# Kernel tuning notes

Hardware: AMD Instinct MI355X
Metric: run time of the kernel (lower is better)

## Reference

```python
import jax
import jax.numpy as jnp
import numpy as np

DEPTH = 8
CODEBOOK_SIZE = 1024
EMBED_DIM = 256
N_TOKENS = 131072


def setup_inputs() -> dict:
    key = jax.random.key(0)
    k_lat, k_cb = jax.random.split(key)
    latent = jax.random.normal(k_lat, (N_TOKENS, EMBED_DIM), dtype=jnp.float32)
    # matches torch.randn(depth, K, D) * 0.02 initialization
    codebooks = jax.random.normal(k_cb, (DEPTH, CODEBOOK_SIZE, EMBED_DIM), dtype=jnp.float32) * 0.02
    return {"latent": latent, "codebooks": codebooks}


def reference(latent, codebooks):
    """Residual VQ: per level, squared-L2 nearest codeword, gather, residual update.

    latent:    [N, D]
    codebooks: [depth, K, D]
    returns (straight_through [N, D], codes [depth, N] int32)
    """

    def step(carry, cb):
        residual, qsum = carry  # [N, D], [N, D]
        # ||r||^2 - 2 r.c + ||c||^2  -> [N, K]
        dist = (
            jnp.sum(residual * residual, axis=-1, keepdims=True)
            - 2.0 * jnp.einsum("nd,kd->nk", residual, cb)
            + jnp.sum(cb * cb, axis=-1)[None, :]
        )
        idx = jnp.argmin(dist, axis=1)  # [N]
        quantized = cb[idx]  # [N, D]
        return (residual - quantized, qsum + quantized), idx

    init = (latent, jnp.zeros_like(latent))
    (_, quantized_sum), codes = jax.lax.scan(step, init, codebooks)
    straight_through = latent + jax.lax.stop_gradient(quantized_sum - latent)
    return straight_through, codes
```

## Files before the change

### kernel.cpp

```cpp
#include <hip/hip_runtime.h>


#define NTOK 131072
#define DEPTH 8
#define KCB 1024
#define DIM 256
#define TM 16
#define RP 260
#define RBP 264
#define WWIN 0.12f
#define ALARM 0.05f
#define LCAP 64

typedef __attribute__((ext_vector_type(8))) short short8v;
typedef __attribute__((ext_vector_type(4))) float f32x4;

__device__ __forceinline__ unsigned short f32_to_bf16_rne(float f) {
  unsigned int u = __float_as_uint(f);
  return (unsigned short)((u + 0x7FFFu + ((u >> 16) & 1u)) >> 16);
}

__device__ __forceinline__ unsigned int fkey(float f) {
  unsigned int b = __float_as_uint(f);
  return (b & 0x80000000u) ? ~b : (b | 0x80000000u);
}
__device__ __forceinline__ float finv(unsigned int k) {
  return (k & 0x80000000u) ? __uint_as_float(k ^ 0x80000000u)
                           : __uint_as_float(~k);
}

__device__ __forceinline__ float np_sumsq_128(const float* p) {
  float s[16];
#pragma unroll
  for (int l = 0; l < 16; ++l) {
    float r0 = __fadd_rn(__fmul_rn(p[l], p[l]),
                         __fmul_rn(p[l + 64], p[l + 64]));
    float r1 = __fadd_rn(__fmul_rn(p[l + 16], p[l + 16]),
                         __fmul_rn(p[l + 80], p[l + 80]));
    float r2 = __fadd_rn(__fmul_rn(p[l + 32], p[l + 32]),
                         __fmul_rn(p[l + 96], p[l + 96]));
    float r3 = __fadd_rn(__fmul_rn(p[l + 48], p[l + 48]),
                         __fmul_rn(p[l + 112], p[l + 112]));
    s[l] = __fadd_rn(__fadd_rn(r0, r1), __fadd_rn(r2, r3));
  }
  float t[8];
#pragma unroll
  for (int l = 0; l < 8; ++l) t[l] = __fadd_rn(s[l], s[l + 8]);
  float u[4];
#pragma unroll
  for (int l = 0; l < 4; ++l) u[l] = __fadd_rn(t[l], t[l + 4]);
  return __fadd_rn(__fadd_rn(u[0], u[2]), __fadd_rn(u[1], u[3]));
}

__device__ __forceinline__ float np_sumsq_256(const float* p) {
  return __fadd_rn(np_sumsq_128(p), np_sumsq_128(p + 128));
}

__device__ __forceinline__ float np_sumsq_256_par(const float* p, int kc) {
  float half[2];
#pragma unroll
  for (int h = 0; h < 2; ++h) {
    const float* q = p + h * 128;
    float r0 = __fadd_rn(__fmul_rn(q[kc], q[kc]),
                         __fmul_rn(q[kc + 64], q[kc + 64]));
    float r1 = __fadd_rn(__fmul_rn(q[kc + 16], q[kc + 16]),
                         __fmul_rn(q[kc + 80], q[kc + 80]));
    float r2 = __fadd_rn(__fmul_rn(q[kc + 32], q[kc + 32]),
                         __fmul_rn(q[kc + 96], q[kc + 96]));
    float r3 = __fadd_rn(__fmul_rn(q[kc + 48], q[kc + 48]),
                         __fmul_rn(q[kc + 112], q[kc + 112]));
    float s = __fadd_rn(__fadd_rn(r0, r1), __fadd_rn(r2, r3));
    float t = __fadd_rn(s, __shfl_down(s, 8, 16));
    float u = __fadd_rn(t, __shfl_down(t, 4, 16));
    float v = __fadd_rn(u, __shfl_down(u, 2, 16));
    half[h] = __fadd_rn(v, __shfl_down(v, 1, 16));
  }
  return __fadd_rn(half[0], half[1]);
}

__device__ __forceinline__ float np_dist(const float* rrow, const float* crow,
                                         float A, float C) {
  float dot = 0.f;
#pragma unroll 8
  for (int q = 0; q < 64; ++q) {
    float4 rv = *(const float4*)(rrow + q * 4);
    float4 cv = *(const float4*)(crow + q * 4);
    dot = fmaf(rv.x, cv.x, dot);
    dot = fmaf(rv.y, cv.y, dot);
    dot = fmaf(rv.z, cv.z, dot);
    dot = fmaf(rv.w, cv.w, dot);
  }
  return __fadd_rn(__fsub_rn(A, __fmul_rn(2.0f, dot)), C);
}

__global__ __launch_bounds__(256) void c2_kernel(const float* __restrict__ cbs,
                                                 float* __restrict__ C32g) {
  int gid = blockIdx.x * 256 + threadIdx.x;
  C32g[gid] = np_sumsq_256(cbs + (size_t)gid * DIM);
}

__global__ __launch_bounds__(256) void pack_kernel(
    const float* __restrict__ cbs, unsigned short* __restrict__ cbf) {
  int gid = blockIdx.x * 256 + threadIdx.x;
  int lane = gid & 63;
  int s = (gid >> 6) & 7;
  int g = (gid >> 9) & 63;
  int lvl = gid >> 15;
  int kcol = g * 16 + (lane & 15);
  int kd0 = s * 32 + (lane >> 4) * 8;
  const float* src = cbs + ((size_t)lvl * KCB + kcol) * DIM + kd0;
  unsigned short t[8];
#pragma unroll
  for (int j = 0; j < 8; ++j) t[j] = f32_to_bf16_rne(src[j]);
  ushort4 lo = {t[0], t[1], t[2], t[3]};
  ushort4 hi = {t[4], t[5], t[6], t[7]};
  *(ushort4*)(cbf + (size_t)gid * 8) = lo;
  *(ushort4*)(cbf + (size_t)gid * 8 + 4) = hi;
}

__global__ __launch_bounds__(256, 6) void rvq_kernel(
    const float* __restrict__ latent, const float* __restrict__ cbs,
    const float* __restrict__ C32g, const unsigned short* __restrict__ cbf,
    float* __restrict__ out) {
  __shared__ float r_m[TM][RP];
  __shared__ __align__(16) unsigned short rb[TM * RBP];
  __shared__ float A_s[TM];
  __shared__ unsigned int gkey[TM];
  __shared__ int cnt[TM];
  __shared__ int list[TM][LCAP];
  __shared__ int idx_s[TM];

  const int tid = threadIdx.x;
  const int w = tid >> 6;
  const int lane = tid & 63;
  const int lc = lane & 15;
  const int lg = lane >> 4;
  const int n0 = blockIdx.x * TM;

  {
    int tok = tid >> 4;
    int db = (tid & 15) * 16;
    const float* src = latent + (size_t)(n0 + tok) * DIM + db;
#pragma unroll
    for (int j = 0; j < 4; ++j) {
      float4 v = *(const float4*)(src + j * 4);
      *(float4*)&r_m[tok][db + j * 4] = v;
      rb[tok * RBP + db + j * 4 + 0] = f32_to_bf16_rne(v.x);
      rb[tok * RBP + db + j * 4 + 1] = f32_to_bf16_rne(v.y);
      rb[tok * RBP + db + j * 4 + 2] = f32_to_bf16_rne(v.z);
      rb[tok * RBP + db + j * 4 + 3] = f32_to_bf16_rne(v.w);
    }
    if (tid < TM) {
      gkey[tid] = 0xFFFFFFFFu;
      cnt[tid] = 0;
    }
  }
  __syncthreads();

  for (int lvl = 0; lvl < DEPTH; ++lvl) {
    const float* cb = cbs + (size_t)lvl * KCB * DIM;

    {
      float A = np_sumsq_256_par(&r_m[tid >> 4][0], tid & 15);
      if ((tid & 15) == 0) A_s[tid >> 4] = A;
    }

#pragma unroll 1
    for (int p = 0; p < 4; ++p) {
      f32x4 acc[4];
#pragma unroll
      for (int nt = 0; nt < 4; ++nt) acc[nt] = (f32x4){0.f, 0.f, 0.f, 0.f};

      const int kt0 = p * 16 + w * 4;
      const unsigned short* bp0 =
          cbf + ((((size_t)lvl * 64 + kt0) * 8) * 64 + lane) * 8;
      short8v a0c = *(const short8v*)&rb[lc * RBP + lg * 8];
      short8v b0c = *(const short8v*)(bp0 + 0 * 4096);
      short8v b1c = *(const short8v*)(bp0 + 1 * 4096);
      short8v b2c = *(const short8v*)(bp0 + 2 * 4096);
      short8v b3c = *(const short8v*)(bp0 + 3 * 4096);
#pragma unroll
      for (int s = 0; s < 8; ++s) {
        short8v a0n, b0n, b1n, b2n, b3n;
        if (s < 7) {
          a0n = *(const short8v*)&rb[lc * RBP + (s + 1) * 32 + lg * 8];
          const unsigned short* bs = bp0 + (size_t)(s + 1) * 512;
          b0n = *(const short8v*)(bs + 0 * 4096);
          b1n = *(const short8v*)(bs + 1 * 4096);
          b2n = *(const short8v*)(bs + 2 * 4096);
          b3n = *(const short8v*)(bs + 3 * 4096);
        }
        acc[0] = __builtin_amdgcn_mfma_f32_16x16x32_bf16(a0c, b0c, acc[0], 0, 0, 0);
        acc[1] = __builtin_amdgcn_mfma_f32_16x16x32_bf16(a0c, b1c, acc[1], 0, 0, 0);
        acc[2] = __builtin_amdgcn_mfma_f32_16x16x32_bf16(a0c, b2c, acc[2], 0, 0, 0);
        acc[3] = __builtin_amdgcn_mfma_f32_16x16x32_bf16(a0c, b3c, acc[3], 0, 0, 0);
        if (s < 7) {
          a0c = a0n;
          b0c = b0n;
          b1c = b1n;
          b2c = b2n;
          b3c = b3n;
        }
      }

      float tmin[4];
#pragma unroll
      for (int reg = 0; reg < 4; ++reg) tmin[reg] = 3.4e38f;
#pragma unroll
      for (int nt = 0; nt < 4; ++nt) {
        float Cv = C32g[lvl * KCB + (kt0 + nt) * 16 + lc];
        f32x4 sc;
#pragma unroll
        for (int reg = 0; reg < 4; ++reg) {
          float v = __fsub_rn(Cv, __fmul_rn(2.0f, acc[nt][reg]));
          sc[reg] = v;
          tmin[reg] = fminf(tmin[reg], v);
        }
        acc[nt] = sc;
      }
#pragma unroll
      for (int m = 1; m <= 8; m <<= 1)
#pragma unroll
        for (int reg = 0; reg < 4; ++reg)
          tmin[reg] = fminf(tmin[reg], __shfl_xor(tmin[reg], m));
      if (lc == 0) {
#pragma unroll
        for (int reg = 0; reg < 4; ++reg)
          atomicMin(&gkey[lg * 4 + reg], fkey(tmin[reg]));
      }
#pragma unroll
      for (int reg = 0; reg < 4; ++reg) {
        int t = lg * 4 + reg;
        float th = finv(gkey[t]) + WWIN;
#pragma unroll
        for (int nt = 0; nt < 4; ++nt) {
          if (acc[nt][reg] <= th) {
            int slot = atomicAdd(&cnt[t], 1);
            if (slot < LCAP) list[t][slot] = (kt0 + nt) * 16 + lc;
          }
        }
      }
    }
    __syncthreads();

    {
      int t = tid >> 4;
      int kc = tid & 15;
      float A = A_s[t];
      float gminf = finv(gkey[t]);
      int n = cnt[t];
      float bd = 3.4e38f;
      int bk = KCB;
      if (n <= LCAP) {
        for (int ci = kc; ci < n; ci += 16) {
          int k = list[t][ci];
          float d = np_dist(&r_m[t][0], cb + (size_t)k * DIM, A,
                            C32g[lvl * KCB + k]);
          if (d < bd || (d == bd && k < bk)) {
            bd = d;
            bk = k;
          }
        }
      }
#pragma unroll
      for (int m = 1; m <= 8; m <<= 1) {
        float od = __shfl_xor(bd, m);
        int ok = __shfl_xor(bk, m);
        if (od < bd || (od == bd && ok < bk)) {
          bd = od;
          bk = ok;
        }
      }
      bool redo =
          (n > LCAP) || (fabsf(__fsub_rn(bd, A) - gminf) > (WWIN - ALARM));
      if (redo) {
        bd = 3.4e38f;
        bk = KCB;
        for (int k = kc; k < KCB; k += 16) {
          float d = np_dist(&r_m[t][0], cb + (size_t)k * DIM, A,
                            C32g[lvl * KCB + k]);
          if (d < bd || (d == bd && k < bk)) {
            bd = d;
            bk = k;
          }
        }
#pragma unroll
        for (int m = 1; m <= 8; m <<= 1) {
          float od = __shfl_xor(bd, m);
          int ok = __shfl_xor(bk, m);
          if (od < bd || (od == bd && ok < bk)) {
            bd = od;
            bk = ok;
          }
        }
      }
      if (kc == 0) {
        idx_s[t] = bk;
        out[(size_t)NTOK * DIM + (size_t)lvl * NTOK + n0 + t] = (float)bk;
      }
    }
    __syncthreads();

    {
      int tok = tid >> 4;
      int db = (tid & 15) * 16;
      const float* crow = cb + (size_t)idx_s[tok] * DIM + db;
#pragma unroll
      for (int j = 0; j < 4; ++j) {
        float4 cv4 = *(const float4*)(crow + j * 4);
        int d = db + j * 4;
        float x0 = __fsub_rn(r_m[tok][d + 0], cv4.x);
        float x1 = __fsub_rn(r_m[tok][d + 1], cv4.y);
        float x2 = __fsub_rn(r_m[tok][d + 2], cv4.z);
        float x3 = __fsub_rn(r_m[tok][d + 3], cv4.w);
        r_m[tok][d + 0] = x0;
        r_m[tok][d + 1] = x1;
        r_m[tok][d + 2] = x2;
        r_m[tok][d + 3] = x3;
        rb[tok * RBP + d + 0] = f32_to_bf16_rne(x0);
        rb[tok * RBP + d + 1] = f32_to_bf16_rne(x1);
        rb[tok * RBP + d + 2] = f32_to_bf16_rne(x2);
        rb[tok * RBP + d + 3] = f32_to_bf16_rne(x3);
      }
      if (tid < TM) {
        gkey[tid] = 0xFFFFFFFFu;
        cnt[tid] = 0;
      }
    }
    __syncthreads();
  }

  {
    int tok = tid >> 4;
    int db = (tid & 15) * 16;
#pragma unroll
    for (int j = 0; j < 4; ++j) {
      int d = db + j * 4;
      size_t gi = (size_t)(n0 + tok) * DIM + d;
      float4 l4 = *(const float4*)(latent + gi);
      float4 qv;
      float q;
      q = __fsub_rn(l4.x, r_m[tok][d + 0]);
      qv.x = __fadd_rn(l4.x, __fsub_rn(q, l4.x));
      q = __fsub_rn(l4.y, r_m[tok][d + 1]);
      qv.y = __fadd_rn(l4.y, __fsub_rn(q, l4.y));
      q = __fsub_rn(l4.z, r_m[tok][d + 2]);
      qv.z = __fadd_rn(l4.z, __fsub_rn(q, l4.z));
      q = __fsub_rn(l4.w, r_m[tok][d + 3]);
      qv.w = __fadd_rn(l4.w, __fsub_rn(q, l4.w));
      *(float4*)(out + gi) = qv;
    }
  }
}

extern "C" void kernel_launch(void* const* d_in, const int* in_sizes, int n_in,
                              void* d_out, int out_size, void* d_ws,
                              size_t ws_size, hipStream_t stream) {
  const float* latent = (const float*)d_in[0];
  const float* codebooks = (const float*)d_in[1];
  float* out = (float*)d_out;
  float* C32g = (float*)d_ws;
  unsigned short* cbf = (unsigned short*)((char*)d_ws + 32768);

  hipLaunchKernelGGL(c2_kernel, dim3(DEPTH * KCB / 256), dim3(256), 0, stream,
                     codebooks, C32g);
  hipLaunchKernelGGL(pack_kernel, dim3(DEPTH * 64 * 8 * 64 / 256), dim3(256),
                     0, stream, codebooks, cbf);
  hipLaunchKernelGGL(rvq_kernel, dim3(NTOK / TM), dim3(256), 0, stream, latent,
                     codebooks, C32g, cbf, out);
}
```

Measured before the change: 2.002 ms.

## Enlarge token tile to 64 and keep bf16 residual fragments in registers

Each block now handles 64 tokens, one 16-token row tile per wave, and each wave sweeps the whole codebook. Before, each wave covered a quarter of the codebook for 16 tokens. Every bf16 codebook fragment loaded from global memory now feeds four times as many tokens, which cuts codebook traffic per token. The shared bf16 residual buffer is removed, and each wave converts its A fragments from the fp32 residual straight into registers once per level. In exchange, occupancy drops (launch bounds go from 6 to 4), register pressure rises from the eight persistent A fragments, and the candidate list cap is reduced to 24, which may send more tokens to the overflow fallback path.

```diff
diff --git a/kernel.cpp b/kernel.cpp
--- a/kernel.cpp
+++ b/kernel.cpp
@@ -5,12 +5,11 @@
 #define DEPTH 8
 #define KCB 1024
 #define DIM 256
-#define TM 16
+#define TM 64
 #define RP 260
-#define RBP 264
 #define WWIN 0.12f
 #define ALARM 0.05f
-#define LCAP 64
+#define LCAP 24
 
 typedef __attribute__((ext_vector_type(8))) short short8v;
 typedef __attribute__((ext_vector_type(4))) float f32x4;
@@ -118,12 +117,11 @@
   *(ushort4*)(cbf + (size_t)gid * 8 + 4) = hi;
 }
 
-__global__ __launch_bounds__(256, 6) void rvq_kernel(
+__global__ __launch_bounds__(256, 4) void rvq_kernel(
     const float* __restrict__ latent, const float* __restrict__ cbs,
     const float* __restrict__ C32g, const unsigned short* __restrict__ cbf,
     float* __restrict__ out) {
   __shared__ float r_m[TM][RP];
-  __shared__ __align__(16) unsigned short rb[TM * RBP];
   __shared__ float A_s[TM];
   __shared__ unsigned int gkey[TM];
   __shared__ int cnt[TM];
@@ -136,20 +134,15 @@
   const int lc = lane & 15;
   const int lg = lane >> 4;
   const int n0 = blockIdx.x * TM;
+  const int mrow = w * 16 + lc;
 
   {
-    int tok = tid >> 4;
-    int db = (tid & 15) * 16;
-    const float* src = latent + (size_t)(n0 + tok) * DIM + db;
-#pragma unroll
-    for (int j = 0; j < 4; ++j) {
-      float4 v = *(const float4*)(src + j * 4);
-      *(float4*)&r_m[tok][db + j * 4] = v;
-      rb[tok * RBP + db + j * 4 + 0] = f32_to_bf16_rne(v.x);
-      rb[tok * RBP + db + j * 4 + 1] = f32_to_bf16_rne(v.y);
-      rb[tok * RBP + db + j * 4 + 2] = f32_to_bf16_rne(v.z);
-      rb[tok * RBP + db + j * 4 + 3] = f32_to_bf16_rne(v.w);
-    }
+    int tok = tid >> 2;
+    int part = tid & 3;
+    const float* src = latent + (size_t)(n0 + tok) * DIM + part * 64;
+#pragma unroll
+    for (int j = 0; j < 16; ++j)
+      *(float4*)&r_m[tok][part * 64 + j * 4] = *(const float4*)(src + j * 4);
     if (tid < TM) {
       gkey[tid] = 0xFFFFFFFFu;
       cnt[tid] = 0;
@@ -160,42 +153,57 @@
   for (int lvl = 0; lvl < DEPTH; ++lvl) {
     const float* cb = cbs + (size_t)lvl * KCB * DIM;
 
-    {
-      float A = np_sumsq_256_par(&r_m[tid >> 4][0], tid & 15);
-      if ((tid & 15) == 0) A_s[tid >> 4] = A;
-    }
+#pragma unroll
+    for (int tb = 0; tb < 4; ++tb) {
+      int t = tb * 16 + (tid >> 4);
+      float A = np_sumsq_256_par(&r_m[t][0], tid & 15);
+      if ((tid & 15) == 0) A_s[t] = A;
+    }
+
+    short8v afr[8];
+#pragma unroll
+    for (int s = 0; s < 8; ++s) {
+      unsigned short tmp[8];
+#pragma unroll
+      for (int j = 0; j < 8; ++j)
+        tmp[j] = f32_to_bf16_rne(r_m[mrow][s * 32 + lg * 8 + j]);
+      afr[s] = (short8v){(short)tmp[0], (short)tmp[1], (short)tmp[2],
+                         (short)tmp[3], (short)tmp[4], (short)tmp[5],
+                         (short)tmp[6], (short)tmp[7]};
+    }
+
+    const unsigned short* bp = cbf + (size_t)lvl * 262144 + lane * 8;
+    f32x4 acc[4];
+#pragma unroll
+    for (int nt = 0; nt < 4; ++nt) acc[nt] = (f32x4){0.f, 0.f, 0.f, 0.f};
+    short8v b0c = *(const short8v*)(bp + 0 * 4096);
+    short8v b1c = *(const short8v*)(bp + 1 * 4096);
+    short8v b2c = *(const short8v*)(bp + 2 * 4096);
+    short8v b3c = *(const short8v*)(bp + 3 * 4096);
 
 #pragma unroll 1
-    for (int p = 0; p < 4; ++p) {
-      f32x4 acc[4];
-#pragma unroll
-      for (int nt = 0; nt < 4; ++nt) acc[nt] = (f32x4){0.f, 0.f, 0.f, 0.f};
-
-      const int kt0 = p * 16 + w * 4;
-      const unsigned short* bp0 =
-          cbf + ((((size_t)lvl * 64 + kt0) * 8) * 64 + lane) * 8;
-      short8v a0c = *(const short8v*)&rb[lc * RBP + lg * 8];
-      short8v b0c = *(const short8v*)(bp0 + 0 * 4096);
-      short8v b1c = *(const short8v*)(bp0 + 1 * 4096);
-      short8v b2c = *(const short8v*)(bp0 + 2 * 4096);
-      short8v b3c = *(const short8v*)(bp0 + 3 * 4096);
+    for (int pass = 0; pass < 16; ++pass) {
 #pragma unroll
       for (int s = 0; s < 8; ++s) {
-        short8v a0n, b0n, b1n, b2n, b3n;
-        if (s < 7) {
-          a0n = *(const short8v*)&rb[lc * RBP + (s + 1) * 32 + lg * 8];
-          const unsigned short* bs = bp0 + (size_t)(s + 1) * 512;
-          b0n = *(const short8v*)(bs + 0 * 4096);
-          b1n = *(const short8v*)(bs + 1 * 4096);
-          b2n = *(const short8v*)(bs + 2 * 4096);
-          b3n = *(const short8v*)(bs + 3 * 4096);
-        }
-        acc[0] = __builtin_amdgcn_mfma_f32_16x16x32_bf16(a0c, b0c, acc[0], 0, 0, 0);
-        acc[1] = __builtin_amdgcn_mfma_f32_16x16x32_bf16(a0c, b1c, acc[1], 0, 0, 0);
-        acc[2] = __builtin_amdgcn_mfma_f32_16x16x32_bf16(a0c, b2c, acc[2], 0, 0, 0);
-        acc[3] = __builtin_amdgcn_mfma_f32_16x16x32_bf16(a0c, b3c, acc[3], 0, 0, 0);
-        if (s < 7) {
-          a0c = a0n;
+        short8v b0n, b1n, b2n, b3n;
+        const bool pf = (s < 7) || (pass < 15);
+        if (pf) {
+          const unsigned short* bn =
+              (s < 7) ? (bp + (s + 1) * 512) : (bp + 16384);
+          b0n = *(const short8v*)(bn + 0 * 4096);
+          b1n = *(const short8v*)(bn + 1 * 4096);
+          b2n = *(const short8v*)(bn + 2 * 4096);
+          b3n = *(const short8v*)(bn + 3 * 4096);
+        }
+        acc[0] =
+            __builtin_amdgcn_mfma_f32_16x16x32_bf16(afr[s], b0c, acc[0], 0, 0, 0);
+        acc[1] =
+            __builtin_amdgcn_mfma_f32_16x16x32_bf16(afr[s], b1c, acc[1], 0, 0, 0);
+        acc[2] =
+            __builtin_amdgcn_mfma_f32_16x16x32_bf16(afr[s], b2c, acc[2], 0, 0, 0);
+        acc[3] =
+            __builtin_amdgcn_mfma_f32_16x16x32_bf16(afr[s], b3c, acc[3], 0, 0, 0);
+        if (pf) {
           b0c = b0n;
           b1c = b1n;
           b2c = b2n;
@@ -208,7 +216,7 @@
       for (int reg = 0; reg < 4; ++reg) tmin[reg] = 3.4e38f;
 #pragma unroll
       for (int nt = 0; nt < 4; ++nt) {
-        float Cv = C32g[lvl * KCB + (kt0 + nt) * 16 + lc];
+        float Cv = C32g[lvl * KCB + (pass * 4 + nt) * 16 + lc];
         f32x4 sc;
 #pragma unroll
         for (int reg = 0; reg < 4; ++reg) {
@@ -226,25 +234,29 @@
       if (lc == 0) {
 #pragma unroll
         for (int reg = 0; reg < 4; ++reg)
-          atomicMin(&gkey[lg * 4 + reg], fkey(tmin[reg]));
+          atomicMin(&gkey[w * 16 + lg * 4 + reg], fkey(tmin[reg]));
       }
 #pragma unroll
       for (int reg = 0; reg < 4; ++reg) {
-        int t = lg * 4 + reg;
+        int t = w * 16 + lg * 4 + reg;
         float th = finv(gkey[t]) + WWIN;
 #pragma unroll
         for (int nt = 0; nt < 4; ++nt) {
           if (acc[nt][reg] <= th) {
             int slot = atomicAdd(&cnt[t], 1);
-            if (slot < LCAP) list[t][slot] = (kt0 + nt) * 16 + lc;
+            if (slot < LCAP) list[t][slot] = (pass * 4 + nt) * 16 + lc;
           }
         }
       }
+#pragma unroll
+      for (int nt = 0; nt < 4; ++nt) acc[nt] = (f32x4){0.f, 0.f, 0.f, 0.f};
+      bp += 16384;
     }
     __syncthreads();
 
-    {
-      int t = tid >> 4;
+#pragma unroll 1
+    for (int tb = 0; tb < 4; ++tb) {
+      int t = tb * 16 + (tid >> 4);
       int kc = tid & 15;
       float A = A_s[t];
       float gminf = finv(gkey[t]);
@@ -301,41 +313,34 @@
     }
     __syncthreads();
 
-    {
-      int tok = tid >> 4;
+#pragma unroll
+    for (int tb = 0; tb < 4; ++tb) {
+      int tok = tb * 16 + (tid >> 4);
       int db = (tid & 15) * 16;
       const float* crow = cb + (size_t)idx_s[tok] * DIM + db;
 #pragma unroll
       for (int j = 0; j < 4; ++j) {
         float4 cv4 = *(const float4*)(crow + j * 4);
         int d = db + j * 4;
-        float x0 = __fsub_rn(r_m[tok][d + 0], cv4.x);
-        float x1 = __fsub_rn(r_m[tok][d + 1], cv4.y);
-        float x2 = __fsub_rn(r_m[tok][d + 2], cv4.z);
-        float x3 = __fsub_rn(r_m[tok][d + 3], cv4.w);
-        r_m[tok][d + 0] = x0;
-        r_m[tok][d + 1] = x1;
-        r_m[tok][d + 2] = x2;
-        r_m[tok][d + 3] = x3;
-        rb[tok * RBP + d + 0] = f32_to_bf16_rne(x0);
-        rb[tok * RBP + d + 1] = f32_to_bf16_rne(x1);
-        rb[tok * RBP + d + 2] = f32_to_bf16_rne(x2);
-        rb[tok * RBP + d + 3] = f32_to_bf16_rne(x3);
-      }
-      if (tid < TM) {
-        gkey[tid] = 0xFFFFFFFFu;
-        cnt[tid] = 0;
-      }
+        r_m[tok][d + 0] = __fsub_rn(r_m[tok][d + 0], cv4.x);
+        r_m[tok][d + 1] = __fsub_rn(r_m[tok][d + 1], cv4.y);
+        r_m[tok][d + 2] = __fsub_rn(r_m[tok][d + 2], cv4.z);
+        r_m[tok][d + 3] = __fsub_rn(r_m[tok][d + 3], cv4.w);
+      }
+    }
+    if (tid < TM) {
+      gkey[tid] = 0xFFFFFFFFu;
+      cnt[tid] = 0;
     }
     __syncthreads();
   }
 
   {
-    int tok = tid >> 4;
-    int db = (tid & 15) * 16;
-#pragma unroll
-    for (int j = 0; j < 4; ++j) {
-      int d = db + j * 4;
+    int tok = tid >> 2;
+    int part = tid & 3;
+#pragma unroll
+    for (int j = 0; j < 16; ++j) {
+      int d = part * 64 + j * 4;
       size_t gi = (size_t)(n0 + tok) * DIM + d;
       float4 l4 = *(const float4*)(latent + gi);
       float4 qv;
```

After: 2.931 ms. 1.46x slower.

## Double tokens per block so each codebook fragment feeds two MFMA row tiles

Applied to the files above, without the earlier changes.

Raises the token tile from 16 to 32 rows per block, so every bf16 codebook fragment loaded from global memory is used by two 16-row MFMA tiles. This halves codebook traffic per token. The k-tile assignment per wave changes to contiguous chunks, and the load, refine and residual-update phases are remapped to 32 tokens. The cost is more registers and LDS per block, with launch bounds cut from 6 to 4 blocks per CU, and half as many blocks in the grid.

```diff
diff --git a/kernel.cpp b/kernel.cpp
--- a/kernel.cpp
+++ b/kernel.cpp
@@ -5,7 +5,7 @@
 #define DEPTH 8
 #define KCB 1024
 #define DIM 256
-#define TM 16
+#define TM 32
 #define RP 260
 #define RBP 264
 #define WWIN 0.12f
@@ -118,7 +118,7 @@
   *(ushort4*)(cbf + (size_t)gid * 8 + 4) = hi;
 }
 
-__global__ __launch_bounds__(256, 6) void rvq_kernel(
+__global__ __launch_bounds__(256, 4) void rvq_kernel(
     const float* __restrict__ latent, const float* __restrict__ cbs,
     const float* __restrict__ C32g, const unsigned short* __restrict__ cbf,
     float* __restrict__ out) {
@@ -138,12 +138,11 @@
   const int n0 = blockIdx.x * TM;
 
   {
-    int tok = tid >> 4;
-    int db = (tid & 15) * 16;
-    const float* src = latent + (size_t)(n0 + tok) * DIM + db;
-#pragma unroll
-    for (int j = 0; j < 4; ++j) {
-      float4 v = *(const float4*)(src + j * 4);
+    int tok = tid >> 3;
+    int db = (tid & 7) * 32;
+#pragma unroll
+    for (int j = 0; j < 8; ++j) {
+      float4 v = *(const float4*)(latent + (size_t)(n0 + tok) * DIM + db + j * 4);
       *(float4*)&r_m[tok][db + j * 4] = v;
       rb[tok * RBP + db + j * 4 + 0] = f32_to_bf16_rne(v.x);
       rb[tok * RBP + db + j * 4 + 1] = f32_to_bf16_rne(v.y);
@@ -160,42 +159,53 @@
   for (int lvl = 0; lvl < DEPTH; ++lvl) {
     const float* cb = cbs + (size_t)lvl * KCB * DIM;
 
-    {
-      float A = np_sumsq_256_par(&r_m[tid >> 4][0], tid & 15);
-      if ((tid & 15) == 0) A_s[tid >> 4] = A;
+#pragma unroll
+    for (int tb = 0; tb < 2; ++tb) {
+      int t = tb * 16 + (tid >> 4);
+      float A = np_sumsq_256_par(&r_m[t][0], tid & 15);
+      if ((tid & 15) == 0) A_s[t] = A;
     }
 
 #pragma unroll 1
     for (int p = 0; p < 4; ++p) {
-      f32x4 acc[4];
-#pragma unroll
-      for (int nt = 0; nt < 4; ++nt) acc[nt] = (f32x4){0.f, 0.f, 0.f, 0.f};
-
-      const int kt0 = p * 16 + w * 4;
+      f32x4 acc[2][4];
+#pragma unroll
+      for (int mt = 0; mt < 2; ++mt)
+#pragma unroll
+        for (int nt = 0; nt < 4; ++nt) acc[mt][nt] = (f32x4){0.f, 0.f, 0.f, 0.f};
+
+      const int kt0 = w * 16 + p * 4;
       const unsigned short* bp0 =
           cbf + ((((size_t)lvl * 64 + kt0) * 8) * 64 + lane) * 8;
       short8v a0c = *(const short8v*)&rb[lc * RBP + lg * 8];
+      short8v a1c = *(const short8v*)&rb[(16 + lc) * RBP + lg * 8];
       short8v b0c = *(const short8v*)(bp0 + 0 * 4096);
       short8v b1c = *(const short8v*)(bp0 + 1 * 4096);
       short8v b2c = *(const short8v*)(bp0 + 2 * 4096);
       short8v b3c = *(const short8v*)(bp0 + 3 * 4096);
 #pragma unroll
       for (int s = 0; s < 8; ++s) {
-        short8v a0n, b0n, b1n, b2n, b3n;
+        short8v a0n, a1n, b0n, b1n, b2n, b3n;
         if (s < 7) {
           a0n = *(const short8v*)&rb[lc * RBP + (s + 1) * 32 + lg * 8];
+          a1n = *(const short8v*)&rb[(16 + lc) * RBP + (s + 1) * 32 + lg * 8];
           const unsigned short* bs = bp0 + (size_t)(s + 1) * 512;
           b0n = *(const short8v*)(bs + 0 * 4096);
           b1n = *(const short8v*)(bs + 1 * 4096);
           b2n = *(const short8v*)(bs + 2 * 4096);
           b3n = *(const short8v*)(bs + 3 * 4096);
         }
-        acc[0] = __builtin_amdgcn_mfma_f32_16x16x32_bf16(a0c, b0c, acc[0], 0, 0, 0);
-        acc[1] = __builtin_amdgcn_mfma_f32_16x16x32_bf16(a0c, b1c, acc[1], 0, 0, 0);
-        acc[2] = __builtin_amdgcn_mfma_f32_16x16x32_bf16(a0c, b2c, acc[2], 0, 0, 0);
-        acc[3] = __builtin_amdgcn_mfma_f32_16x16x32_bf16(a0c, b3c, acc[3], 0, 0, 0);
+        acc[0][0] = __builtin_amdgcn_mfma_f32_16x16x32_bf16(a0c, b0c, acc[0][0], 0, 0, 0);
+        acc[0][1] = __builtin_amdgcn_mfma_f32_16x16x32_bf16(a0c, b1c, acc[0][1], 0, 0, 0);
+        acc[0][2] = __builtin_amdgcn_mfma_f32_16x16x32_bf16(a0c, b2c, acc[0][2], 0, 0, 0);
+        acc[0][3] = __builtin_amdgcn_mfma_f32_16x16x32_bf16(a0c, b3c, acc[0][3], 0, 0, 0);
+        acc[1][0] = __builtin_amdgcn_mfma_f32_16x16x32_bf16(a1c, b0c, acc[1][0], 0, 0, 0);
+        acc[1][1] = __builtin_amdgcn_mfma_f32_16x16x32_bf16(a1c, b1c, acc[1][1], 0, 0, 0);
+        acc[1][2] = __builtin_amdgcn_mfma_f32_16x16x32_bf16(a1c, b2c, acc[1][2], 0, 0, 0);
+        acc[1][3] = __builtin_amdgcn_mfma_f32_16x16x32_bf16(a1c, b3c, acc[1][3], 0, 0, 0);
         if (s < 7) {
           a0c = a0n;
+          a1c = a1n;
           b0c = b0n;
           b1c = b1n;
           b2c = b2n;
@@ -203,48 +213,60 @@
         }
       }
 
-      float tmin[4];
-#pragma unroll
-      for (int reg = 0; reg < 4; ++reg) tmin[reg] = 3.4e38f;
+      float tmin[2][4];
+#pragma unroll
+      for (int mt = 0; mt < 2; ++mt)
+#pragma unroll
+        for (int reg = 0; reg < 4; ++reg) tmin[mt][reg] = 3.4e38f;
 #pragma unroll
       for (int nt = 0; nt < 4; ++nt) {
         float Cv = C32g[lvl * KCB + (kt0 + nt) * 16 + lc];
-        f32x4 sc;
+#pragma unroll
+        for (int mt = 0; mt < 2; ++mt) {
+          f32x4 sc;
+#pragma unroll
+          for (int reg = 0; reg < 4; ++reg) {
+            float v = __fsub_rn(Cv, __fmul_rn(2.0f, acc[mt][nt][reg]));
+            sc[reg] = v;
+            tmin[mt][reg] = fminf(tmin[mt][reg], v);
+          }
+          acc[mt][nt] = sc;
+        }
+      }
+#pragma unroll
+      for (int m = 1; m <= 8; m <<= 1)
+#pragma unroll
+        for (int mt = 0; mt < 2; ++mt)
+#pragma unroll
+          for (int reg = 0; reg < 4; ++reg)
+            tmin[mt][reg] = fminf(tmin[mt][reg], __shfl_xor(tmin[mt][reg], m));
+      if (lc == 0) {
+#pragma unroll
+        for (int mt = 0; mt < 2; ++mt)
+#pragma unroll
+          for (int reg = 0; reg < 4; ++reg)
+            atomicMin(&gkey[mt * 16 + lg * 4 + reg], fkey(tmin[mt][reg]));
+      }
+#pragma unroll
+      for (int mt = 0; mt < 2; ++mt)
 #pragma unroll
         for (int reg = 0; reg < 4; ++reg) {
-          float v = __fsub_rn(Cv, __fmul_rn(2.0f, acc[nt][reg]));
-          sc[reg] = v;
-          tmin[reg] = fminf(tmin[reg], v);
-        }
-        acc[nt] = sc;
-      }
-#pragma unroll
-      for (int m = 1; m <= 8; m <<= 1)
-#pragma unroll
-        for (int reg = 0; reg < 4; ++reg)
-          tmin[reg] = fminf(tmin[reg], __shfl_xor(tmin[reg], m));
-      if (lc == 0) {
-#pragma unroll
-        for (int reg = 0; reg < 4; ++reg)
-          atomicMin(&gkey[lg * 4 + reg], fkey(tmin[reg]));
-      }
-#pragma unroll
-      for (int reg = 0; reg < 4; ++reg) {
-        int t = lg * 4 + reg;
-        float th = finv(gkey[t]) + WWIN;
-#pragma unroll
-        for (int nt = 0; nt < 4; ++nt) {
-          if (acc[nt][reg] <= th) {
-            int slot = atomicAdd(&cnt[t], 1);
-            if (slot < LCAP) list[t][slot] = (kt0 + nt) * 16 + lc;
-          }
-        }
-      }
+          int t = mt * 16 + lg * 4 + reg;
+          float th = finv(gkey[t]) + WWIN;
+#pragma unroll
+          for (int nt = 0; nt < 4; ++nt) {
+            if (acc[mt][nt][reg] <= th) {
+              int slot = atomicAdd(&cnt[t], 1);
+              if (slot < LCAP) list[t][slot] = (kt0 + nt) * 16 + lc;
+            }
+          }
+        }
     }
     __syncthreads();
 
-    {
-      int t = tid >> 4;
+#pragma unroll 1
+    for (int tb = 0; tb < 2; ++tb) {
+      int t = tb * 16 + (tid >> 4);
       int kc = tid & 15;
       float A = A_s[t];
       float gminf = finv(gkey[t]);
@@ -302,11 +324,11 @@
     __syncthreads();
 
     {
-      int tok = tid >> 4;
-      int db = (tid & 15) * 16;
+      int tok = tid >> 3;
+      int db = (tid & 7) * 32;
       const float* crow = cb + (size_t)idx_s[tok] * DIM + db;
 #pragma unroll
-      for (int j = 0; j < 4; ++j) {
+      for (int j = 0; j < 8; ++j) {
         float4 cv4 = *(const float4*)(crow + j * 4);
         int d = db + j * 4;
         float x0 = __fsub_rn(r_m[tok][d + 0], cv4.x);
@@ -331,10 +353,10 @@
   }
 
   {
-    int tok = tid >> 4;
-    int db = (tid & 15) * 16;
-#pragma unroll
-    for (int j = 0; j < 4; ++j) {
+    int tok = tid >> 3;
+    int db = (tid & 7) * 32;
+#pragma unroll
+    for (int j = 0; j < 8; ++j) {
       int d = db + j * 4;
       size_t gi = (size_t)(n0 + tok) * DIM + d;
       float4 l4 = *(const float4*)(latent + gi);
```

Measured after the change: 1.987 ms. Within noise of the previous version (-0.8%).

## Stream bf16 codebook tiles through per-wave LDS ring with async global-to-LDS loads

Applied to the files above, without the earlier changes.

Replaces direct global loads of codebook fragments with a 6-deep per-wave LDS ring filled by global_load_lds, using explicit vmcnt/lgkmcnt waits and sched barriers to overlap loads with MFMA. Each wave now owns 16 contiguous k-tiles processed two at a time, with the A operand held in registers (converted from fp32 residual once per level) instead of a shared bf16 copy. The goal is to hide global memory latency for the codebook stream. It costs 48KB of LDS plus more registers, so launch bounds drop to 4 waves-per-EU, and the hand-tuned wait counts are fragile.

```diff
diff --git a/kernel.cpp b/kernel.cpp
--- a/kernel.cpp
+++ b/kernel.cpp
@@ -7,13 +7,23 @@
 #define DIM 256
 #define TM 16
 #define RP 260
-#define RBP 264
 #define WWIN 0.12f
 #define ALARM 0.05f
 #define LCAP 64
 
 typedef __attribute__((ext_vector_type(8))) short short8v;
 typedef __attribute__((ext_vector_type(4))) float f32x4;
+
+#define WVM(n) asm volatile("s_waitcnt vmcnt(" #n ")" ::: "memory")
+#define WLK(n) asm volatile("s_waitcnt lgkmcnt(" #n ")" ::: "memory")
+#define SBAR() __builtin_amdgcn_sched_barrier(0)
+
+__device__ __forceinline__ void gload16(const unsigned short* g,
+                                        unsigned short* l) {
+  __builtin_amdgcn_global_load_lds(
+      (__attribute__((address_space(1))) const void*)g,
+      (__attribute__((address_space(3))) void*)l, 16, 0, 0);
+}
 
 __device__ __forceinline__ unsigned short f32_to_bf16_rne(float f) {
   unsigned int u = __float_as_uint(f);
@@ -118,12 +128,12 @@
   *(ushort4*)(cbf + (size_t)gid * 8 + 4) = hi;
 }
 
-__global__ __launch_bounds__(256, 6) void rvq_kernel(
+__global__ __launch_bounds__(256, 4) void rvq_kernel(
     const float* __restrict__ latent, const float* __restrict__ cbs,
     const float* __restrict__ C32g, const unsigned short* __restrict__ cbf,
     float* __restrict__ out) {
   __shared__ float r_m[TM][RP];
-  __shared__ __align__(16) unsigned short rb[TM * RBP];
+  __shared__ __align__(16) unsigned short ringS[4][6144];
   __shared__ float A_s[TM];
   __shared__ unsigned int gkey[TM];
   __shared__ int cnt[TM];
@@ -142,14 +152,8 @@
     int db = (tid & 15) * 16;
     const float* src = latent + (size_t)(n0 + tok) * DIM + db;
 #pragma unroll
-    for (int j = 0; j < 4; ++j) {
-      float4 v = *(const float4*)(src + j * 4);
-      *(float4*)&r_m[tok][db + j * 4] = v;
-      rb[tok * RBP + db + j * 4 + 0] = f32_to_bf16_rne(v.x);
-      rb[tok * RBP + db + j * 4 + 1] = f32_to_bf16_rne(v.y);
-      rb[tok * RBP + db + j * 4 + 2] = f32_to_bf16_rne(v.z);
-      rb[tok * RBP + db + j * 4 + 3] = f32_to_bf16_rne(v.w);
-    }
+    for (int j = 0; j < 4; ++j)
+      *(float4*)&r_m[tok][db + j * 4] = *(const float4*)(src + j * 4);
     if (tid < TM) {
       gkey[tid] = 0xFFFFFFFFu;
       cnt[tid] = 0;
@@ -165,79 +169,122 @@
       if ((tid & 15) == 0) A_s[tid >> 4] = A;
     }
 
+    short8v afr[8];
+#pragma unroll
+    for (int s = 0; s < 8; ++s) {
+      unsigned short tmp[8];
+#pragma unroll
+      for (int j = 0; j < 8; ++j)
+        tmp[j] = f32_to_bf16_rne(r_m[lc][s * 32 + lg * 8 + j]);
+      afr[s] = (short8v){(short)tmp[0], (short)tmp[1], (short)tmp[2],
+                         (short)tmp[3], (short)tmp[4], (short)tmp[5],
+                         (short)tmp[6], (short)tmp[7]};
+    }
+
+    unsigned short* ring = &ringS[w][0];
+    const unsigned short* cbase = cbf + ((size_t)lvl * 64 + w * 16) * 4096;
+
+    f32x4 acc[2];
+    acc[0] = (f32x4){0.f, 0.f, 0.f, 0.f};
+    acc[1] = (f32x4){0.f, 0.f, 0.f, 0.f};
+
+#pragma unroll
+    for (int q = 0; q < 6; ++q) {
+      const unsigned short* g0 = cbase + (q << 9) + lane * 8;
+      gload16(g0, ring + q * 1024);
+      gload16(g0 + 4096, ring + q * 1024 + 512);
+    }
+    WVM(10);
+    SBAR();
+    short8v bA0 = *(const short8v*)(ring + lane * 8);
+    short8v bA1 = *(const short8v*)(ring + 512 + lane * 8);
+    int rs = 1;
+    int is = 0;
+
 #pragma unroll 1
-    for (int p = 0; p < 4; ++p) {
-      f32x4 acc[4];
-#pragma unroll
-      for (int nt = 0; nt < 4; ++nt) acc[nt] = (f32x4){0.f, 0.f, 0.f, 0.f};
-
-      const int kt0 = p * 16 + w * 4;
-      const unsigned short* bp0 =
-          cbf + ((((size_t)lvl * 64 + kt0) * 8) * 64 + lane) * 8;
-      short8v a0c = *(const short8v*)&rb[lc * RBP + lg * 8];
-      short8v b0c = *(const short8v*)(bp0 + 0 * 4096);
-      short8v b1c = *(const short8v*)(bp0 + 1 * 4096);
-      short8v b2c = *(const short8v*)(bp0 + 2 * 4096);
-      short8v b3c = *(const short8v*)(bp0 + 3 * 4096);
+    for (int p = 0; p < 8; ++p) {
 #pragma unroll
       for (int s = 0; s < 8; ++s) {
-        short8v a0n, b0n, b1n, b2n, b3n;
-        if (s < 7) {
-          a0n = *(const short8v*)&rb[lc * RBP + (s + 1) * 32 + lg * 8];
-          const unsigned short* bs = bp0 + (size_t)(s + 1) * 512;
-          b0n = *(const short8v*)(bs + 0 * 4096);
-          b1n = *(const short8v*)(bs + 1 * 4096);
-          b2n = *(const short8v*)(bs + 2 * 4096);
-          b3n = *(const short8v*)(bs + 3 * 4096);
-        }
-        acc[0] = __builtin_amdgcn_mfma_f32_16x16x32_bf16(a0c, b0c, acc[0], 0, 0, 0);
-        acc[1] = __builtin_amdgcn_mfma_f32_16x16x32_bf16(a0c, b1c, acc[1], 0, 0, 0);
-        acc[2] = __builtin_amdgcn_mfma_f32_16x16x32_bf16(a0c, b2c, acc[2], 0, 0, 0);
-        acc[3] = __builtin_amdgcn_mfma_f32_16x16x32_bf16(a0c, b3c, acc[3], 0, 0, 0);
-        if (s < 7) {
-          a0c = a0n;
-          b0c = b0n;
-          b1c = b1n;
-          b2c = b2n;
-          b3c = b3n;
-        }
-      }
-
-      float tmin[4];
-#pragma unroll
-      for (int reg = 0; reg < 4; ++reg) tmin[reg] = 3.4e38f;
-#pragma unroll
-      for (int nt = 0; nt < 4; ++nt) {
-        float Cv = C32g[lvl * KCB + (kt0 + nt) * 16 + lc];
-        f32x4 sc;
-#pragma unroll
-        for (int reg = 0; reg < 4; ++reg) {
-          float v = __fsub_rn(Cv, __fmul_rn(2.0f, acc[nt][reg]));
-          sc[reg] = v;
-          tmin[reg] = fminf(tmin[reg], v);
-        }
-        acc[nt] = sc;
-      }
-#pragma unroll
-      for (int m = 1; m <= 8; m <<= 1)
-#pragma unroll
-        for (int reg = 0; reg < 4; ++reg)
-          tmin[reg] = fminf(tmin[reg], __shfl_xor(tmin[reg], m));
-      if (lc == 0) {
-#pragma unroll
-        for (int reg = 0; reg < 4; ++reg)
-          atomicMin(&gkey[lg * 4 + reg], fkey(tmin[reg]));
-      }
-#pragma unroll
-      for (int reg = 0; reg < 4; ++reg) {
-        int t = lg * 4 + reg;
-        float th = finv(gkey[t]) + WWIN;
-#pragma unroll
-        for (int nt = 0; nt < 4; ++nt) {
-          if (acc[nt][reg] <= th) {
-            int slot = atomicAdd(&cnt[t], 1);
-            if (slot < LCAP) list[t][slot] = (kt0 + nt) * 16 + lc;
-          }
+        acc[0] =
+            __builtin_amdgcn_mfma_f32_16x16x32_bf16(afr[s], bA0, acc[0], 0, 0, 0);
+        acc[1] =
+            __builtin_amdgcn_mfma_f32_16x16x32_bf16(afr[s], bA1, acc[1], 0, 0, 0);
+        SBAR();
+        const int idx = p * 8 + s;
+        if (idx < 63) {
+          if (p < 7) {
+            WVM(8);
+          } else {
+            if (s <= 2) {
+              WVM(8);
+            } else if (s == 3) {
+              WVM(6);
+            } else if (s == 4) {
+              WVM(4);
+            } else if (s == 5) {
+              WVM(2);
+            } else {
+              WVM(0);
+            }
+          }
+          SBAR();
+          short8v nb0 = *(const short8v*)(ring + rs * 1024 + lane * 8);
+          short8v nb1 = *(const short8v*)(ring + rs * 1024 + 512 + lane * 8);
+          rs = (rs == 5) ? 0 : rs + 1;
+          if (idx + 6 < 64) {
+            WLK(2);
+            SBAR();
+            const int n = idx + 6;
+            const unsigned short* g0 =
+                cbase + ((((n >> 3) * 16 + (n & 7)) << 9)) + lane * 8;
+            gload16(g0, ring + is * 1024);
+            gload16(g0 + 4096, ring + is * 1024 + 512);
+            is = (is == 5) ? 0 : is + 1;
+          }
+          bA0 = nb0;
+          bA1 = nb1;
+        }
+        if (s == 7) {
+          float tmin[4];
+          f32x4 sv[2];
+#pragma unroll
+          for (int reg = 0; reg < 4; ++reg) tmin[reg] = 3.4e38f;
+#pragma unroll
+          for (int f = 0; f < 2; ++f) {
+            float Cv = C32g[lvl * KCB + (w * 16 + p * 2 + f) * 16 + lc];
+            f32x4 sc;
+#pragma unroll
+            for (int reg = 0; reg < 4; ++reg) {
+              float v = __fsub_rn(Cv, __fmul_rn(2.0f, acc[f][reg]));
+              sc[reg] = v;
+              tmin[reg] = fminf(tmin[reg], v);
+            }
+            sv[f] = sc;
+          }
+#pragma unroll
+          for (int m = 1; m <= 8; m <<= 1)
+#pragma unroll
+            for (int reg = 0; reg < 4; ++reg)
+              tmin[reg] = fminf(tmin[reg], __shfl_xor(tmin[reg], m));
+          if (lc == 0) {
+#pragma unroll
+            for (int reg = 0; reg < 4; ++reg)
+              atomicMin(&gkey[lg * 4 + reg], fkey(tmin[reg]));
+          }
+#pragma unroll
+          for (int f = 0; f < 2; ++f)
+#pragma unroll
+            for (int reg = 0; reg < 4; ++reg) {
+              int t = lg * 4 + reg;
+              float th = finv(gkey[t]) + WWIN;
+              if (sv[f][reg] <= th) {
+                int slot = atomicAdd(&cnt[t], 1);
+                if (slot < LCAP)
+                  list[t][slot] = (w * 16 + p * 2 + f) * 16 + lc;
+              }
+            }
+          acc[0] = (f32x4){0.f, 0.f, 0.f, 0.f};
+          acc[1] = (f32x4){0.f, 0.f, 0.f, 0.f};
         }
       }
     }
@@ -309,18 +356,10 @@
       for (int j = 0; j < 4; ++j) {
         float4 cv4 = *(const float4*)(crow + j * 4);
         int d = db + j * 4;
-        float x0 = __fsub_rn(r_m[tok][d + 0], cv4.x);
-        float x1 = __fsub_rn(r_m[tok][d + 1], cv4.y);
-        float x2 = __fsub_rn(r_m[tok][d + 2], cv4.z);
-        float x3 = __fsub_rn(r_m[tok][d + 3], cv4.w);
-        r_m[tok][d + 0] = x0;
-        r_m[tok][d + 1] = x1;
-        r_m[tok][d + 2] = x2;
-        r_m[tok][d + 3] = x3;
-        rb[tok * RBP + d + 0] = f32_to_bf16_rne(x0);
-        rb[tok * RBP + d + 1] = f32_to_bf16_rne(x1);
-        rb[tok * RBP + d + 2] = f32_to_bf16_rne(x2);
-        rb[tok * RBP + d + 3] = f32_to_bf16_rne(x3);
+        r_m[tok][d + 0] = __fsub_rn(r_m[tok][d + 0], cv4.x);
+        r_m[tok][d + 1] = __fsub_rn(r_m[tok][d + 1], cv4.y);
+        r_m[tok][d + 2] = __fsub_rn(r_m[tok][d + 2], cv4.z);
+        r_m[tok][d + 3] = __fsub_rn(r_m[tok][d + 3], cv4.w);
       }
       if (tid < TM) {
         gkey[tid] = 0xFFFFFFFFu;
```

Result: slower. 4.430 ms (+121.3%).
